# Performance work log

Measured on AMD Instinct MI355X. Metric: run time of the kernel, lower is better.

## Reference

```python
import jax, jax.numpy as jnp
import numpy as np

NUM_CLASSES = 19
IGNORE_INDEX = -1


def setup_inputs() -> dict:
    key = jax.random.key(0)
    k1, k2 = jax.random.split(key)
    pred_label = jax.random.normal(k1, (8, NUM_CLASSES, 512, 1024), dtype=jnp.float32)
    label = jax.random.randint(k2, (8, 512, 1024), 0, NUM_CLASSES, dtype=jnp.int64)
    return {"pred_label": pred_label, "label": label}


def reference(pred_label, label):
    # argmax over class dim -> [B, H, W]
    pred = jnp.argmax(pred_label, axis=1)
    p = pred.reshape(-1)
    l = label.reshape(-1)
    valid = (l != IGNORE_INDEX).astype(jnp.float32)
    # clip label so ignore entries index a real bin; their weight is zero anyway
    lc = jnp.clip(l, 0, NUM_CLASSES - 1)
    # batched bincounts replace the per-image histc loop: all images summed at once
    area_label = jnp.bincount(lc, weights=valid, length=NUM_CLASSES)
    area_pred = jnp.bincount(p, weights=valid, length=NUM_CLASSES)
    inter_w = valid * (p == l).astype(jnp.float32)
    area_intersect = jnp.bincount(lc, weights=inter_w, length=NUM_CLASSES)
    area_union = area_pred + area_label - area_intersect
    iou = area_intersect / area_union  # 0/0 -> nan, matching torch/numpy
    result = jnp.nanmean(iou)
    result = jnp.where(jnp.isnan(result), jnp.float32(0.5), result)
    return 1.0 - result
```

## Files before the change

kernel.cpp:

```cpp
#include <hip/hip_runtime.h>

#define NUM_CLASSES 19
#define IGNORE_INDEX (-1)
#define BATCH 8
#define HW (512 * 1024)
#define NPIX (BATCH * HW)
#define NGROUP (NPIX / 4)
#define NBINS (3 * NUM_CLASSES)

__global__ __launch_bounds__(256) void iou_hist_kernel(
    const float* __restrict__ pred,
    const int* __restrict__ label,
    unsigned int* __restrict__ ghist)
{
    __shared__ unsigned int h[4][NBINS];
    const int tid = threadIdx.x;
    const int wid = tid >> 6;

    for (int i = tid; i < 4 * NBINS; i += 256) ((unsigned int*)h)[i] = 0u;
    __syncthreads();

    unsigned int* __restrict__ hw_ = h[wid];

    const int stride = gridDim.x * 256;
    for (int g = blockIdx.x * 256 + tid; g < NGROUP; g += stride) {
        const int p  = g << 2;
        const int b  = p >> 19;
        const int hw = p & (HW - 1);

        const float* bp = pred + (long)b * (long)(NUM_CLASSES * (long)HW) + hw;
        float4 best = *(const float4*)bp;
        int bcx = 0, bcy = 0, bcz = 0, bcw = 0;
#pragma unroll
        for (int c = 1; c < NUM_CLASSES; ++c) {
            bp += HW;
            const float4 v = *(const float4*)bp;
            if (v.x > best.x) { best.x = v.x; bcx = c; }
            if (v.y > best.y) { best.y = v.y; bcy = c; }
            if (v.z > best.z) { best.z = v.z; bcz = c; }
            if (v.w > best.w) { best.w = v.w; bcw = c; }
        }

        const int4 lab = ((const int4*)label)[g];

        {
            const int l = lab.x;
            if (l != IGNORE_INDEX) {
                const int lc = min(max(l, 0), NUM_CLASSES - 1);
                atomicAdd(&hw_[lc], 1u);
                atomicAdd(&hw_[NUM_CLASSES + bcx], 1u);
                if (bcx == l) atomicAdd(&hw_[2 * NUM_CLASSES + lc], 1u);
            }
        }
        {
            const int l = lab.y;
            if (l != IGNORE_INDEX) {
                const int lc = min(max(l, 0), NUM_CLASSES - 1);
                atomicAdd(&hw_[lc], 1u);
                atomicAdd(&hw_[NUM_CLASSES + bcy], 1u);
                if (bcy == l) atomicAdd(&hw_[2 * NUM_CLASSES + lc], 1u);
            }
        }
        {
            const int l = lab.z;
            if (l != IGNORE_INDEX) {
                const int lc = min(max(l, 0), NUM_CLASSES - 1);
                atomicAdd(&hw_[lc], 1u);
                atomicAdd(&hw_[NUM_CLASSES + bcz], 1u);
                if (bcz == l) atomicAdd(&hw_[2 * NUM_CLASSES + lc], 1u);
            }
        }
        {
            const int l = lab.w;
            if (l != IGNORE_INDEX) {
                const int lc = min(max(l, 0), NUM_CLASSES - 1);
                atomicAdd(&hw_[lc], 1u);
                atomicAdd(&hw_[NUM_CLASSES + bcw], 1u);
                if (bcw == l) atomicAdd(&hw_[2 * NUM_CLASSES + lc], 1u);
            }
        }
    }

    __syncthreads();
    for (int i = tid; i < NBINS; i += 256) {
        const unsigned int s = h[0][i] + h[1][i] + h[2][i] + h[3][i];
        if (s) atomicAdd(&ghist[i], s);
    }
}

__global__ void iou_finish_kernel(const unsigned int* __restrict__ ghist,
                                  float* __restrict__ out)
{
    if (threadIdx.x == 0 && blockIdx.x == 0) {
        float sum = 0.0f;
        int cnt = 0;
        for (int c = 0; c < NUM_CLASSES; ++c) {
            const float a_lab = (float)ghist[c];
            const float a_prd = (float)ghist[NUM_CLASSES + c];
            const float a_int = (float)ghist[2 * NUM_CLASSES + c];
            const float a_uni = a_prd + a_lab - a_int;
            if (a_uni > 0.0f) { sum += a_int / a_uni; ++cnt; }
        }
        const float mean = (cnt > 0) ? (sum / (float)cnt) : 0.5f;
        out[0] = 1.0f - mean;
    }
}

extern "C" void kernel_launch(void* const* d_in, const int* in_sizes, int n_in,
                              void* d_out, int out_size, void* d_ws, size_t ws_size,
                              hipStream_t stream)
{
    const float* pred  = (const float*)d_in[0];
    const int*   label = (const int*)d_in[1];
    float*       out   = (float*)d_out;
    unsigned int* ghist = (unsigned int*)d_ws;

    hipMemsetAsync(ghist, 0, NBINS * sizeof(unsigned int), stream);

    iou_hist_kernel<<<1024, 256, 0, stream>>>(pred, label, ghist);
    iou_finish_kernel<<<1, 64, 0, stream>>>(ghist, out);
}
```

Measured before the change: 449.1 us.

## Replace global atomics and memset with per-block partial histograms reduced in finish kernel

Each histogram block now writes its 57 bins, padded to 64, to its own slot in the workspace, instead of atomically adding into a global histogram. A 1024-thread finish kernel sums the 2048 partial histograms through shared memory. The memset launch is dropped and the grid doubles to 2048 blocks. This removes global atomic contention and one launch, at the cost of a larger final reduction pass over about 512 KB of partials.

```diff
diff --git a/kernel.cpp b/kernel.cpp
--- a/kernel.cpp
+++ b/kernel.cpp
@@ -7,11 +7,13 @@
 #define NPIX (BATCH * HW)
 #define NGROUP (NPIX / 4)
 #define NBINS (3 * NUM_CLASSES)
+#define BINS_PAD 64
+#define HBLOCKS 2048
 
 __global__ __launch_bounds__(256) void iou_hist_kernel(
     const float* __restrict__ pred,
     const int* __restrict__ label,
-    unsigned int* __restrict__ ghist)
+    unsigned int* __restrict__ bh)
 {
     __shared__ unsigned int h[4][NBINS];
     const int tid = threadIdx.x;
@@ -22,7 +24,7 @@
 
     unsigned int* __restrict__ hw_ = h[wid];
 
-    const int stride = gridDim.x * 256;
+    const int stride = HBLOCKS * 256;
     for (int g = blockIdx.x * 256 + tid; g < NGROUP; g += stride) {
         const int p  = g << 2;
         const int b  = p >> 19;
@@ -82,22 +84,43 @@
     }
 
     __syncthreads();
-    for (int i = tid; i < NBINS; i += 256) {
-        const unsigned int s = h[0][i] + h[1][i] + h[2][i] + h[3][i];
-        if (s) atomicAdd(&ghist[i], s);
+    unsigned int* __restrict__ outp = bh + (size_t)blockIdx.x * BINS_PAD;
+    for (int i = tid; i < BINS_PAD; i += 256) {
+        const unsigned int s = (i < NBINS)
+            ? (h[0][i] + h[1][i] + h[2][i] + h[3][i]) : 0u;
+        outp[i] = s;
     }
 }
 
-__global__ void iou_finish_kernel(const unsigned int* __restrict__ ghist,
-                                  float* __restrict__ out)
+__global__ __launch_bounds__(1024) void iou_finish_kernel(
+    const unsigned int* __restrict__ bh, float* __restrict__ out)
 {
-    if (threadIdx.x == 0 && blockIdx.x == 0) {
+    __shared__ unsigned int part[16][BINS_PAD];
+    const int tid = threadIdx.x;
+    const int bin = tid & 63;
+    const int row = tid >> 6;
+
+    unsigned int s = 0;
+    for (int b = row; b < HBLOCKS; b += 16)
+        s += bh[(size_t)b * BINS_PAD + bin];
+    part[row][bin] = s;
+    __syncthreads();
+
+    if (tid < BINS_PAD) {
+        unsigned int t = 0;
+#pragma unroll
+        for (int r = 0; r < 16; ++r) t += part[r][tid];
+        part[0][tid] = t;
+    }
+    __syncthreads();
+
+    if (tid == 0) {
         float sum = 0.0f;
         int cnt = 0;
         for (int c = 0; c < NUM_CLASSES; ++c) {
-            const float a_lab = (float)ghist[c];
-            const float a_prd = (float)ghist[NUM_CLASSES + c];
-            const float a_int = (float)ghist[2 * NUM_CLASSES + c];
+            const float a_lab = (float)part[0][c];
+            const float a_prd = (float)part[0][NUM_CLASSES + c];
+            const float a_int = (float)part[0][2 * NUM_CLASSES + c];
             const float a_uni = a_prd + a_lab - a_int;
             if (a_uni > 0.0f) { sum += a_int / a_uni; ++cnt; }
         }
@@ -113,10 +136,8 @@
     const float* pred  = (const float*)d_in[0];
     const int*   label = (const int*)d_in[1];
     float*       out   = (float*)d_out;
-    unsigned int* ghist = (unsigned int*)d_ws;
+    unsigned int* bh   = (unsigned int*)d_ws;
 
-    hipMemsetAsync(ghist, 0, NBINS * sizeof(unsigned int), stream);
-
-    iou_hist_kernel<<<1024, 256, 0, stream>>>(pred, label, ghist);
-    iou_finish_kernel<<<1, 64, 0, stream>>>(ghist, out);
+    iou_hist_kernel<<<HBLOCKS, 256, 0, stream>>>(pred, label, bh);
+    iou_finish_kernel<<<1, 1024, 0, stream>>>(bh, out);
 }
```

Measured after the change: 449.2 us. No clear change (+0.0%).
